# Kernel optimization log

Hardware: AMD Instinct MI355X
Metric: run time of the kernel (lower is better)

Reference implementation:

```python
import jax, jax.numpy as jnp
import numpy as np

N = 10000       # num nodes
E = 320000      # num edges
F_IN = 500      # num_features
HID = 64        # hidden
C = 10          # num_classes (width of propagated signal)
RANK = 3
K = 10          # Chebyshev hops


def setup_inputs() -> dict:
    key = jax.random.key(0)
    ks = jax.random.split(key, 10)
    feature = jax.random.normal(ks[0], (N, F_IN), jnp.float32)
    src = jax.random.randint(ks[1], (E,), 0, N)
    dst = jax.random.randint(ks[2], (E,), 0, N)
    edges = jnp.stack([src, dst]).astype(jnp.int64)
    CTC = jax.random.normal(ks[3], (N, N), jnp.float32) * 0.01
    W1 = jax.random.normal(ks[4], (F_IN, HID), jnp.float32) / np.sqrt(F_IN)
    b1 = jnp.zeros((HID,), jnp.float32)
    W2 = jax.random.normal(ks[5], (HID, C), jnp.float32) / np.sqrt(HID)
    b2 = jnp.zeros((C,), jnp.float32)
    gamma = jax.random.normal(ks[6], (RANK, K + 1), jnp.float32)   # Parameter gamma
    Wp = jax.random.normal(ks[7], (K + 1, C, RANK), jnp.float32) / np.sqrt(C)  # proj_list weights (transposed)
    bp = jnp.zeros((K + 1, RANK), jnp.float32)
    return dict(feature=feature, edges=edges, CTC=CTC, W1=W1, b1=b1,
                W2=W2, b2=b2, gamma=gamma, Wp=Wp, bp=bp)


def _cheb_norm(src, dst, num_nodes):
    # remove self loops (mask to zero weight: jit-safe, mathematically identical)
    w = jnp.where(src == dst, 0.0, 1.0).astype(jnp.float32)
    deg = jax.ops.segment_sum(w, src, num_segments=num_nodes)
    dinv = jnp.where(deg > 0, 1.0 / jnp.sqrt(jnp.maximum(deg, 1e-30)), 0.0)
    # sym-normalized Laplacian: off-diag = -D^-1/2 A D^-1/2, diag = 1
    w_off = -dinv[src] * w * dinv[dst]
    lam = 2.0 * jnp.maximum(jnp.max(w_off), 1.0)  # lambda_max = 2*max(L weights); diag ones dominate
    w_off = 2.0 * w_off / lam
    diag = 2.0 / lam - 1.0  # scaled diag (2*1/lam) plus fill_value=-1 self loop, summed by scatter-add
    return w_off, diag


def reference(feature, edges, CTC, W1, b1, W2, b2, gamma, Wp, bp):
    # MLP (dropout is identity in eval mode)
    x = jax.nn.relu(feature @ W1 + b1)
    x = x @ W2 + b2  # (N, C)
    num_nodes = x.shape[0]
    src, dst = edges[0], edges[1]
    w_off, diag = _cheb_norm(src, dst, num_nodes)

    def prop(t):  # scatter-add message passing: out[i] = sum_j L_hat[i,j] t[j]
        return jax.ops.segment_sum(w_off[:, None] * t[src], dst,
                                   num_segments=num_nodes) + diag * t

    def eta(Txk, k):  # gated low-rank mixing coefficient per node
        h = jnp.tanh(Txk @ Wp[k] + bp[k])        # (N, rank)
        e = (h @ gamma[:, k]) / RANK             # (N,)
        return CTC @ e                           # (N,)

    Tx0 = x
    Tx1 = prop(Tx0)
    hidden = Tx0 * eta(Tx0, 0)[:, None] + Tx1 * eta(Tx1, 1)[:, None]
    for k in range(1, K):
        Tx2 = 2.0 * prop(Tx1) - Tx0
        Tx0, Tx1 = Tx1, Tx2
        hidden = hidden + Tx1 * eta(Tx1, k + 1)[:, None]
    return jax.nn.log_softmax(hidden, axis=1)
```

## Files before the change

kernel.cpp:

```cpp
#include <hip/hip_runtime.h>
#include <hip/hip_bf16.h>
#include <math.h>

#define NNODES 10000
#define NEDGES 320000
#define FIN    500
#define HIDN   64
#define NC     10
#define RANKP  3
#define KHOP   10
#define KP1    11

__global__ __launch_bounds__(256) void mlp_kernel(
    const float* __restrict__ feature, const float* __restrict__ W1,
    const float* __restrict__ b1, const float* __restrict__ W2,
    const float* __restrict__ b2, float* __restrict__ Tx0) {
  __shared__ float feat[4][FIN];
  __shared__ float hid[4][HIDN];
  const int t = threadIdx.x;
  const int n = t >> 6;
  const int h = t & 63;
  const int i0 = blockIdx.x * 4;

  for (int idx = t; idx < 4 * FIN; idx += 256) {
    int nn = idx / FIN, f = idx - nn * FIN;
    feat[nn][f] = feature[(size_t)(i0 + nn) * FIN + f];
  }
  __syncthreads();

  float acc = b1[h];
#pragma unroll 4
  for (int f = 0; f < FIN; ++f)
    acc = fmaf(feat[n][f], W1[f * HIDN + h], acc);
  hid[n][h] = fmaxf(acc, 0.f);
  __syncthreads();

  if (h < NC) {
    float a2 = b2[h];
#pragma unroll
    for (int k = 0; k < HIDN; ++k)
      a2 = fmaf(hid[n][k], W2[k * NC + h], a2);
    Tx0[(size_t)(i0 + n) * NC + h] = a2;
  }
}


__global__ void degcnt_kernel(const int* __restrict__ src, const int* __restrict__ dst,
                              float* __restrict__ deg, int* __restrict__ cnt) {
  int e = blockIdx.x * 256 + threadIdx.x;
  if (e >= NEDGES) return;
  int s = src[e], d = dst[e];
  if (s != d) {
    atomicAdd(&deg[s], 1.0f);
    atomicAdd(&cnt[d], 1);
  }
}

__global__ __launch_bounds__(256) void scan_kernel(const int* __restrict__ cnt,
                                                   int* __restrict__ row_start,
                                                   int* __restrict__ cursor) {
  const int t = threadIdx.x, lane = t & 63, w = t >> 6;
  const int CH = 40;
  const int base = t * CH;
  int sum = 0;
  for (int j = 0; j < CH; ++j) {
    int idx = base + j;
    if (idx < NNODES) sum += cnt[idx];
  }
  int inc = sum;
#pragma unroll
  for (int d = 1; d < 64; d <<= 1) {
    int u = __shfl_up(inc, d);
    if (lane >= d) inc += u;
  }
  __shared__ int wtot[4];
  if (lane == 63) wtot[w] = inc;
  __syncthreads();
  int add = 0;
  for (int i = 0; i < 4; ++i)
    if (i < w) add += wtot[i];
  int run = add + inc - sum;
  for (int j = 0; j < CH; ++j) {
    int idx = base + j;
    if (idx < NNODES) {
      int v = cnt[idx];
      row_start[idx] = run;
      cursor[idx] = run;
      run += v;
    }
  }
  if (t == 255) row_start[NNODES] = run;
}

__global__ void fill_kernel(const int* __restrict__ src, const int* __restrict__ dst,
                            const float* __restrict__ deg, int* __restrict__ cursor,
                            int2* __restrict__ packed) {
  int e = blockIdx.x * 256 + threadIdx.x;
  if (e >= NEDGES) return;
  int s = src[e], d = dst[e];
  if (s == d) return;
  float ds_ = deg[s], dd = deg[d];
  float dis = (ds_ > 0.f) ? 1.0f / sqrtf(ds_) : 0.f;
  float did = (dd  > 0.f) ? 1.0f / sqrtf(dd)  : 0.f;
  float w = -dis * did;
  int slot = atomicAdd(&cursor[d], 1);
  packed[slot] = make_int2(s, __float_as_int(w));
}

__global__ __launch_bounds__(256) void gather_kernel(
    const int* __restrict__ row_start, const int2* __restrict__ packed,
    const float* __restrict__ tin, const float* __restrict__ sub,
    float* __restrict__ tout, float scale) {
  const int g    = (blockIdx.x * 256 + threadIdx.x) >> 4;
  const int lane = threadIdx.x & 15;
  if (g >= NNODES) return;
  const int s0 = row_start[g], s1 = row_start[g + 1];
  float acc[NC];
#pragma unroll
  for (int c = 0; c < NC; ++c) acc[c] = 0.f;
  for (int j = s0 + lane; j < s1; j += 16) {
    int2 p = packed[j];
    float w = __int_as_float(p.y);
    const float2* t2 = (const float2*)(tin + (size_t)p.x * NC);
    float2 a0 = t2[0], a1 = t2[1], a2 = t2[2], a3 = t2[3], a4 = t2[4];
    acc[0] = fmaf(w, a0.x, acc[0]); acc[1] = fmaf(w, a0.y, acc[1]);
    acc[2] = fmaf(w, a1.x, acc[2]); acc[3] = fmaf(w, a1.y, acc[3]);
    acc[4] = fmaf(w, a2.x, acc[4]); acc[5] = fmaf(w, a2.y, acc[5]);
    acc[6] = fmaf(w, a3.x, acc[6]); acc[7] = fmaf(w, a3.y, acc[7]);
    acc[8] = fmaf(w, a4.x, acc[8]); acc[9] = fmaf(w, a4.y, acc[9]);
  }
#pragma unroll
  for (int c = 0; c < NC; ++c) {
    float v = acc[c];
#pragma unroll
    for (int off = 8; off > 0; off >>= 1) v += __shfl_xor(v, off);
    acc[c] = v;
  }
  if (lane == 0) {
    float* to = tout + (size_t)g * NC;
    if (sub) {
      const float* sb = sub + (size_t)g * NC;
#pragma unroll
      for (int c = 0; c < NC; ++c) to[c] = fmaf(scale, acc[c], -sb[c]);
    } else {
#pragma unroll
      for (int c = 0; c < NC; ++c) to[c] = scale * acc[c];
    }
  }
}

__global__ void proj_kernel(const float* __restrict__ Txall, const float* __restrict__ Wp,
                            const float* __restrict__ bp, const float* __restrict__ gamma,
                            float* __restrict__ Emat) {
  int idx = blockIdx.x * 256 + threadIdx.x;
  if (idx >= NNODES * KP1) return;
  const int k = idx / NNODES, i = idx - k * NNODES;
  const float* tx = Txall + ((size_t)k * NNODES + i) * NC;
  float tv[NC];
#pragma unroll
  for (int c = 0; c < NC; ++c) tv[c] = tx[c];
  float e = 0.f;
#pragma unroll
  for (int r = 0; r < RANKP; ++r) {
    float hh = bp[k * RANKP + r];
#pragma unroll
    for (int c = 0; c < NC; ++c)
      hh = fmaf(tv[c], Wp[(k * NC + c) * RANKP + r], hh);
    e = fmaf(tanhf(hh), gamma[r * KP1 + k], e);
  }
  Emat[(size_t)k * NNODES + i] = e * (1.0f / RANKP);
}

__global__ __launch_bounds__(256) void gemv_final_kernel(
    const float* __restrict__ CTC, const float* __restrict__ Emat,
    const float* __restrict__ Txall, float* __restrict__ out) {
  const int i0 = blockIdx.x * 4;
  const int t = threadIdx.x;
  float acc[4][KP1];
#pragma unroll
  for (int r = 0; r < 4; ++r)
#pragma unroll
    for (int k = 0; k < KP1; ++k) acc[r][k] = 0.f;

  const int n4 = NNODES / 4;
  for (int j4 = t; j4 < n4; j4 += 256) {
    float4 ev[KP1];
#pragma unroll
    for (int k = 0; k < KP1; ++k)
      ev[k] = ((const float4*)(Emat + (size_t)k * NNODES))[j4];
#pragma unroll
    for (int r = 0; r < 4; ++r) {
      float4 cv = ((const float4*)(CTC + (size_t)(i0 + r) * NNODES))[j4];
#pragma unroll
      for (int k = 0; k < KP1; ++k) {
        acc[r][k] = fmaf(cv.x, ev[k].x, acc[r][k]);
        acc[r][k] = fmaf(cv.y, ev[k].y, acc[r][k]);
        acc[r][k] = fmaf(cv.z, ev[k].z, acc[r][k]);
        acc[r][k] = fmaf(cv.w, ev[k].w, acc[r][k]);
      }
    }
  }

#pragma unroll
  for (int r = 0; r < 4; ++r)
#pragma unroll
    for (int k = 0; k < KP1; ++k) {
      float v = acc[r][k];
#pragma unroll
      for (int off = 32; off > 0; off >>= 1) v += __shfl_xor(v, off);
      acc[r][k] = v;
    }
  __shared__ float red[4][4 * KP1];
  const int w = t >> 6, lane = t & 63;
  if (lane == 0) {
#pragma unroll
    for (int r = 0; r < 4; ++r)
#pragma unroll
      for (int k = 0; k < KP1; ++k) red[w][r * KP1 + k] = acc[r][k];
  }
  __syncthreads();
  if (t < 4 * KP1) {
    red[0][t] = red[0][t] + red[1][t] + red[2][t] + red[3][t];
  }
  __syncthreads();
  if (t < 4) {
    const int node = i0 + t;
    float h[NC];
#pragma unroll
    for (int c = 0; c < NC; ++c) h[c] = 0.f;
    for (int k = 0; k < KP1; ++k) {
      const float e = red[0][t * KP1 + k];
      const float* tx = Txall + ((size_t)k * NNODES + node) * NC;
#pragma unroll
      for (int c = 0; c < NC; ++c) h[c] = fmaf(tx[c], e, h[c]);
    }
    float m = h[0];
#pragma unroll
    for (int c = 1; c < NC; ++c) m = fmaxf(m, h[c]);
    float s = 0.f;
#pragma unroll
    for (int c = 0; c < NC; ++c) s += expf(h[c] - m);
    const float ls = logf(s);
#pragma unroll
    for (int c = 0; c < NC; ++c) out[(size_t)node * NC + c] = h[c] - m - ls;
  }
}

extern "C" void kernel_launch(void* const* d_in, const int* in_sizes, int n_in,
                              void* d_out, int out_size, void* d_ws, size_t ws_size,
                              hipStream_t stream) {
  const float* feature = (const float*)d_in[0];
  const int*   edges   = (const int*)d_in[1];
  const float* CTC     = (const float*)d_in[2];
  const float* W1      = (const float*)d_in[3];
  const float* b1      = (const float*)d_in[4];
  const float* W2      = (const float*)d_in[5];
  const float* b2      = (const float*)d_in[6];
  const float* gamma   = (const float*)d_in[7];
  const float* Wp      = (const float*)d_in[8];
  const float* bp      = (const float*)d_in[9];
  const int* src = edges;
  const int* dst = edges + NEDGES;
  float* out = (float*)d_out;

  float* ws        = (float*)d_ws;
  float* Txall     = ws;
  float* deg       = Txall + (size_t)KP1 * NNODES * NC;
  int*   cnt       = (int*)(deg + NNODES);
  int*   row_start = cnt + NNODES;
  int*   cursor    = row_start + NNODES + 8;
  int2*  packed    = (int2*)(cursor + NNODES + 8);
  float* Emat      = (float*)(packed + NEDGES);

  const int EB = (NEDGES + 255) / 256;
  const int GB = (NNODES * 16 + 255) / 256;
  const int PB = (NNODES * KP1 + 255) / 256;

  hipMemsetAsync(deg, 0, 2 * NNODES * sizeof(float), stream);

  mlp_kernel<<<NNODES / 4, 256, 0, stream>>>(feature, W1, b1, W2, b2, Txall);
  degcnt_kernel<<<EB, 256, 0, stream>>>(src, dst, deg, cnt);
  scan_kernel<<<1, 256, 0, stream>>>(cnt, row_start, cursor);
  fill_kernel<<<EB, 256, 0, stream>>>(src, dst, deg, cursor, packed);

  float* Tx0 = Txall;
  float* Tx1 = Txall + (size_t)NNODES * NC;
  gather_kernel<<<GB, 256, 0, stream>>>(row_start, packed, Tx0, nullptr, Tx1, 1.0f);
  for (int k = 1; k < KHOP; ++k) {
    float* prev = Txall + (size_t)(k - 1) * NNODES * NC;
    float* cur  = Txall + (size_t)k * NNODES * NC;
    float* nxt  = Txall + (size_t)(k + 1) * NNODES * NC;
    gather_kernel<<<GB, 256, 0, stream>>>(row_start, packed, cur, prev, nxt, 2.0f);
  }

  proj_kernel<<<PB, 256, 0, stream>>>(Txall, Wp, bp, gamma, Emat);
  gemv_final_kernel<<<NNODES / 4, 256, 0, stream>>>(CTC, Emat, Txall, out);
}
```

Measured before the change: 798.1 us.

## Fuse MLP with degree counting and last gather with projection

Merges the MLP and degree/count kernels into one launch, with block index deciding the role. The MLP part now handles 8 nodes per block, loads features with float4 and splits the inner product into two accumulators. The last Chebyshev gather is fused with the per-node projection/tanh kernel, so each 16-lane group computes all 11 eta values for its node. This removes two launches and one pass over Txall, but the fused projection reads 10 earlier Tx rows per node in a strided pattern.

```diff
diff --git a/kernel.cpp b/kernel.cpp
--- a/kernel.cpp
+++ b/kernel.cpp
@@ -10,49 +10,51 @@
 #define RANKP  3
 #define KHOP   10
 #define KP1    11
-
-__global__ __launch_bounds__(256) void mlp_kernel(
+#define MLPB   (NNODES / 8)
+#define EB     (NEDGES / 256)
+
+__global__ __launch_bounds__(256) void mlp_degcnt_kernel(
     const float* __restrict__ feature, const float* __restrict__ W1,
     const float* __restrict__ b1, const float* __restrict__ W2,
-    const float* __restrict__ b2, float* __restrict__ Tx0) {
-  __shared__ float feat[4][FIN];
-  __shared__ float hid[4][HIDN];
+    const float* __restrict__ b2, const int* __restrict__ src,
+    const int* __restrict__ dst, float* __restrict__ Tx0,
+    float* __restrict__ deg, int* __restrict__ cnt) {
+  __shared__ float feat[8][FIN];
+  __shared__ float hid[8][HIDN + 1];
   const int t = threadIdx.x;
-  const int n = t >> 6;
-  const int h = t & 63;
-  const int i0 = blockIdx.x * 4;
-
-  for (int idx = t; idx < 4 * FIN; idx += 256) {
-    int nn = idx / FIN, f = idx - nn * FIN;
-    feat[nn][f] = feature[(size_t)(i0 + nn) * FIN + f];
-  }
-  __syncthreads();
-
-  float acc = b1[h];
-#pragma unroll 4
-  for (int f = 0; f < FIN; ++f)
-    acc = fmaf(feat[n][f], W1[f * HIDN + h], acc);
-  hid[n][h] = fmaxf(acc, 0.f);
-  __syncthreads();
-
-  if (h < NC) {
-    float a2 = b2[h];
-#pragma unroll
-    for (int k = 0; k < HIDN; ++k)
-      a2 = fmaf(hid[n][k], W2[k * NC + h], a2);
-    Tx0[(size_t)(i0 + n) * NC + h] = a2;
-  }
-}
-
-
-__global__ void degcnt_kernel(const int* __restrict__ src, const int* __restrict__ dst,
-                              float* __restrict__ deg, int* __restrict__ cnt) {
-  int e = blockIdx.x * 256 + threadIdx.x;
-  if (e >= NEDGES) return;
-  int s = src[e], d = dst[e];
-  if (s != d) {
-    atomicAdd(&deg[s], 1.0f);
-    atomicAdd(&cnt[d], 1);
+  if (blockIdx.x < MLPB) {
+    const int i0 = blockIdx.x * 8;
+    const float4* fsrc = (const float4*)(feature + (size_t)i0 * FIN);
+    float4* fdst = (float4*)&feat[0][0];
+    for (int j = t; j < (8 * FIN) / 4; j += 256) fdst[j] = fsrc[j];
+    __syncthreads();
+    const int w = t >> 6, lane = t & 63;
+    for (int nn = w; nn < 8; nn += 4) {
+      float acc0 = b1[lane], acc1 = 0.f;
+      for (int f = 0; f < FIN; f += 2) {
+        acc0 = fmaf(feat[nn][f],     W1[f * HIDN + lane],       acc0);
+        acc1 = fmaf(feat[nn][f + 1], W1[(f + 1) * HIDN + lane], acc1);
+      }
+      hid[nn][lane] = fmaxf(acc0 + acc1, 0.f);
+    }
+    __syncthreads();
+    if (t < 8 * NC) {
+      const int nn = t / NC, c = t - nn * NC;
+      float a2 = b2[c];
+#pragma unroll
+      for (int k2 = 0; k2 < HIDN; ++k2)
+        a2 = fmaf(hid[nn][k2], W2[k2 * NC + c], a2);
+      Tx0[(size_t)(i0 + nn) * NC + c] = a2;
+    }
+  } else {
+    int e = (blockIdx.x - MLPB) * 256 + t;
+    if (e < NEDGES) {
+      int s = src[e], d = dst[e];
+      if (s != d) {
+        atomicAdd(&deg[s], 1.0f);
+        atomicAdd(&cnt[d], 1);
+      }
+    }
   }
 }
 
@@ -149,26 +151,71 @@
   }
 }
 
-__global__ void proj_kernel(const float* __restrict__ Txall, const float* __restrict__ Wp,
-                            const float* __restrict__ bp, const float* __restrict__ gamma,
-                            float* __restrict__ Emat) {
-  int idx = blockIdx.x * 256 + threadIdx.x;
-  if (idx >= NNODES * KP1) return;
-  const int k = idx / NNODES, i = idx - k * NNODES;
-  const float* tx = Txall + ((size_t)k * NNODES + i) * NC;
-  float tv[NC];
-#pragma unroll
-  for (int c = 0; c < NC; ++c) tv[c] = tx[c];
-  float e = 0.f;
-#pragma unroll
-  for (int r = 0; r < RANKP; ++r) {
-    float hh = bp[k * RANKP + r];
-#pragma unroll
-    for (int c = 0; c < NC; ++c)
-      hh = fmaf(tv[c], Wp[(k * NC + c) * RANKP + r], hh);
-    e = fmaf(tanhf(hh), gamma[r * KP1 + k], e);
-  }
-  Emat[(size_t)k * NNODES + i] = e * (1.0f / RANKP);
+__global__ __launch_bounds__(256) void gather_proj_kernel(
+    const int* __restrict__ row_start, const int2* __restrict__ packed,
+    const float* __restrict__ Txall, const float* __restrict__ Wp,
+    const float* __restrict__ bp, const float* __restrict__ gamma,
+    float* __restrict__ Emat) {
+  const int g    = (blockIdx.x * 256 + threadIdx.x) >> 4;
+  const int lane = threadIdx.x & 15;
+  if (g >= NNODES) return;
+  const float* tin = Txall + (size_t)(KHOP - 1) * NNODES * NC;
+  const float* sub = Txall + (size_t)(KHOP - 2) * NNODES * NC;
+  float*       tout = (float*)Txall + (size_t)KHOP * NNODES * NC;
+
+  const int s0 = row_start[g], s1 = row_start[g + 1];
+  float acc[NC];
+#pragma unroll
+  for (int c = 0; c < NC; ++c) acc[c] = 0.f;
+  for (int j = s0 + lane; j < s1; j += 16) {
+    int2 p = packed[j];
+    float w = __int_as_float(p.y);
+    const float2* t2 = (const float2*)(tin + (size_t)p.x * NC);
+    float2 a0 = t2[0], a1 = t2[1], a2 = t2[2], a3 = t2[3], a4 = t2[4];
+    acc[0] = fmaf(w, a0.x, acc[0]); acc[1] = fmaf(w, a0.y, acc[1]);
+    acc[2] = fmaf(w, a1.x, acc[2]); acc[3] = fmaf(w, a1.y, acc[3]);
+    acc[4] = fmaf(w, a2.x, acc[4]); acc[5] = fmaf(w, a2.y, acc[5]);
+    acc[6] = fmaf(w, a3.x, acc[6]); acc[7] = fmaf(w, a3.y, acc[7]);
+    acc[8] = fmaf(w, a4.x, acc[8]); acc[9] = fmaf(w, a4.y, acc[9]);
+  }
+#pragma unroll
+  for (int c = 0; c < NC; ++c) {
+    float v = acc[c];
+#pragma unroll
+    for (int off = 8; off > 0; off >>= 1) v += __shfl_xor(v, off);
+    acc[c] = v;
+  }
+  float r10[NC];
+  const float* sb = sub + (size_t)g * NC;
+#pragma unroll
+  for (int c = 0; c < NC; ++c) r10[c] = fmaf(2.f, acc[c], -sb[c]);
+  if (lane == 0) {
+    float* to = tout + (size_t)g * NC;
+#pragma unroll
+    for (int c = 0; c < NC; ++c) to[c] = r10[c];
+  }
+  if (lane < KP1) {
+    const int k = lane;
+    float tv[NC];
+    if (k < KHOP) {
+      const float* tx = Txall + ((size_t)k * NNODES + g) * NC;
+#pragma unroll
+      for (int c = 0; c < NC; ++c) tv[c] = tx[c];
+    } else {
+#pragma unroll
+      for (int c = 0; c < NC; ++c) tv[c] = r10[c];
+    }
+    float e = 0.f;
+#pragma unroll
+    for (int r = 0; r < RANKP; ++r) {
+      float hh = bp[k * RANKP + r];
+#pragma unroll
+      for (int c = 0; c < NC; ++c)
+        hh = fmaf(tv[c], Wp[(k * NC + c) * RANKP + r], hh);
+      e = fmaf(tanhf(hh), gamma[r * KP1 + k], e);
+    }
+    Emat[(size_t)k * NNODES + g] = e * (1.0f / RANKP);
+  }
 }
 
 __global__ __launch_bounds__(256) void gemv_final_kernel(
@@ -272,27 +319,26 @@
   int2*  packed    = (int2*)(cursor + NNODES + 8);
   float* Emat      = (float*)(packed + NEDGES);
 
-  const int EB = (NEDGES + 255) / 256;
   const int GB = (NNODES * 16 + 255) / 256;
-  const int PB = (NNODES * KP1 + 255) / 256;
 
   hipMemsetAsync(deg, 0, 2 * NNODES * sizeof(float), stream);
 
-  mlp_kernel<<<NNODES / 4, 256, 0, stream>>>(feature, W1, b1, W2, b2, Txall);
-  degcnt_kernel<<<EB, 256, 0, stream>>>(src, dst, deg, cnt);
+  mlp_degcnt_kernel<<<MLPB + EB, 256, 0, stream>>>(feature, W1, b1, W2, b2,
+                                                   src, dst, Txall, deg, cnt);
   scan_kernel<<<1, 256, 0, stream>>>(cnt, row_start, cursor);
   fill_kernel<<<EB, 256, 0, stream>>>(src, dst, deg, cursor, packed);
 
   float* Tx0 = Txall;
   float* Tx1 = Txall + (size_t)NNODES * NC;
   gather_kernel<<<GB, 256, 0, stream>>>(row_start, packed, Tx0, nullptr, Tx1, 1.0f);
-  for (int k = 1; k < KHOP; ++k) {
+  for (int k = 1; k < KHOP - 1; ++k) {
     float* prev = Txall + (size_t)(k - 1) * NNODES * NC;
     float* cur  = Txall + (size_t)k * NNODES * NC;
     float* nxt  = Txall + (size_t)(k + 1) * NNODES * NC;
     gather_kernel<<<GB, 256, 0, stream>>>(row_start, packed, cur, prev, nxt, 2.0f);
   }
-
-  proj_kernel<<<PB, 256, 0, stream>>>(Txall, Wp, bp, gamma, Emat);
+  gather_proj_kernel<<<GB, 256, 0, stream>>>(row_start, packed, Txall, Wp, bp,
+                                             gamma, Emat);
+
   gemv_final_kernel<<<NNODES / 4, 256, 0, stream>>>(CTC, Emat, Txall, out);
 }
```

After: 755.4 us. 5.4% less time.
